# Kernel tuning notes

Hardware: AMD Instinct MI355X
Metric: run time of the kernel (lower is better)

## Reference

```python
import jax, jax.numpy as jnp
import numpy as np

N_NODES = 262144
N_EDGES = 4194304
NUM_GRAPHS = 1024
K = 2          # k clusters / particles
D = 4          # particle_latent_dim
D_Q = D // 2   # position part of latent


def setup_inputs() -> dict:
    key = jax.random.key(0)
    ks = jax.random.split(key, 20)
    w = lambda i, shape: 0.1 * jax.random.normal(ks[i], shape, jnp.float32)
    return {
        "x": jax.random.normal(ks[0], (N_NODES, 4), jnp.float32),
        "pos": jax.random.normal(ks[1], (N_NODES, 3), jnp.float32),
        "edge_index": jax.random.randint(ks[2], (2, N_EDGES), 0, N_NODES),
        "batch": jnp.sort(jax.random.randint(ks[3], (N_NODES,), 0, NUM_GRAPHS)),
        "enc_w1": w(4, (9, 16)), "enc_b1": jnp.zeros((16,), jnp.float32),
        "enc_w2": w(5, (16, 16)), "enc_b2": jnp.zeros((16,), jnp.float32),
        "pool_w": w(6, (16, K)), "pool_b": jnp.zeros((K,), jnp.float32),
        "toz_w": w(7, (16, D)), "toz_b": jnp.zeros((D,), jnp.float32),
        "vp_w1": w(8, (1, 32)), "vp_b1": jnp.zeros((32,), jnp.float32),
        "vp_w2": w(9, (32, 1)), "vp_b2": jnp.zeros((1,), jnp.float32),
        "bridge_w": w(10, (K * D, 8 * 4)), "bridge_b": jnp.zeros((8 * 4,), jnp.float32),
    }


def reference(x, pos, edge_index, batch,
              enc_w1, enc_b1, enc_w2, enc_b2,
              pool_w, pool_b, toz_w, toz_b,
              vp_w1, vp_b1, vp_w2, vp_b2,
              bridge_w, bridge_b):
    src = edge_index[0]  # j (source)
    dst = edge_index[1]  # i (target, PyG default flow)

    # --- EquiLayer: edge gather -> small MLP message -> mean scatter ---
    rel_pos = pos[src] - pos[dst]
    dist = jnp.linalg.norm(rel_pos, axis=-1, keepdims=True)       # [E,1]
    feat = jnp.concatenate([x[dst], x[src], dist], axis=-1)       # [E,9]
    msg = jax.nn.silu(feat @ enc_w1 + enc_b1) @ enc_w2 + enc_b2   # [E,16]
    agg = jax.ops.segment_sum(msg, dst, num_segments=N_NODES)     # [N,16]
    cnt = jax.ops.segment_sum(jnp.ones((msg.shape[0], 1), msg.dtype), dst,
                              num_segments=N_NODES)
    h = jax.nn.relu(agg / jnp.maximum(cnt, 1.0))                  # [N,16]

    # --- softmax-weighted scatter pooling over graphs ---
    s = jax.nn.softmax(h @ pool_w + pool_b, axis=-1)              # [N,K]
    weighted = s[:, :, None] * h[:, None, :]                      # [N,K,16]
    pooled = jax.ops.segment_sum(weighted, batch, num_segments=NUM_GRAPHS)  # [B,K,16]
    z = pooled @ toz_w + toz_b                                    # [B,K,D]

    # --- decode ---
    recon = (z.reshape(z.shape[0], -1) @ bridge_w + bridge_b).reshape(-1, 8, 4)

    # --- pairwise potential + forces on position part of latent ---
    iu0, iu1 = np.triu_indices(K, 1)

    def potential(q):
        diff = q[:, :, None, :] - q[:, None, :, :]
        d = jnp.sqrt(jnp.sum(diff * diff, axis=-1) + 1e-6)        # [B,K,K]
        d_flat = d[:, iu0, iu1][..., None]                        # [B,P,1]
        v = jax.nn.softplus(d_flat @ vp_w1 + vp_b1) @ vp_w2 + vp_b2
        return v.sum(axis=1)                                      # [B,1]

    q = z[..., :D_Q]
    V = potential(q)
    forces = -jax.grad(lambda qq: potential(qq).sum())(q)
    return recon, z, s, forces, V
```

## Files before the change

kernel.cpp:

```cpp
#include <hip/hip_runtime.h>
#include <math.h>

#define N_NODES   262144
#define N_EDGES   4194304
#define NUM_GRAPHS 1024
#define NBKT      256
#define BNODE     1024
#define CAPK      17408
#define NBLK      256
#define EPB       16384
#define SEGCAP    112

typedef _Float16 h8 __attribute__((ext_vector_type(8)));

static __device__ __forceinline__ float fast_rcp(float v) {
    return __builtin_amdgcn_rcpf(v);
}

__global__ __launch_bounds__(1024) void bin_pack_kernel(
    const int* __restrict__ ei, const float* __restrict__ x,
    const float* __restrict__ pos,
    int* __restrict__ cnts, int* __restrict__ staged,
    h8* __restrict__ xp, float* __restrict__ pooled)
{
    __shared__ int cnt[NBKT], rcnt[NBKT], lbase[NBKT];
    __shared__ int wsum[4];
    __shared__ int stage[EPB];
    int tid = threadIdx.x;
    if (tid < NBKT) { cnt[tid] = 0; rcnt[tid] = 0; }
    __syncthreads();

    {
        int n0 = blockIdx.x * 1024 + tid;
        float4 xv = *(const float4*)(x + 4*n0);
        h8 o;
        o[0] = (_Float16)xv.x; o[1] = (_Float16)xv.y;
        o[2] = (_Float16)xv.z; o[3] = (_Float16)xv.w;
        o[4] = (_Float16)pos[3*n0+0]; o[5] = (_Float16)pos[3*n0+1];
        o[6] = (_Float16)pos[3*n0+2]; o[7] = (_Float16)0.0f;
        xp[n0] = o;
        if (blockIdx.x < 32) pooled[blockIdx.x*1024 + tid] = 0.0f;
    }

    int base = blockIdx.x * EPB;
    const int4* d4 = (const int4*)(ei + N_EDGES + base);
    const int4* s4 = (const int4*)(ei + base);
    int4 dv[4];
    #pragma unroll
    for (int i = 0; i < 4; ++i) {
        dv[i] = d4[i*1024 + tid];
        atomicAdd(&cnt[dv[i].x >> 10], 1);
        atomicAdd(&cnt[dv[i].y >> 10], 1);
        atomicAdd(&cnt[dv[i].z >> 10], 1);
        atomicAdd(&cnt[dv[i].w >> 10], 1);
    }
    __syncthreads();

    int lane = tid & 63, wid = tid >> 6;
    if (tid < NBKT) {
        int inc = cnt[tid];
        #pragma unroll
        for (int o = 1; o < 64; o <<= 1) {
            int t = __shfl_up(inc, o);
            if (lane >= o) inc += t;
        }
        if (lane == 63) wsum[wid] = inc;
        cnt[tid] = inc;
    }
    __syncthreads();
    if (tid < NBKT) {
        int inc  = cnt[tid];
        int prev = __shfl_up(inc, 1);
        int excl = (lane == 0) ? 0 : prev;
        int wb = 0;
        #pragma unroll
        for (int w = 0; w < 4; ++w) if (w < wid) wb += wsum[w];
        lbase[tid] = wb + excl;
    }
    __syncthreads();

    #pragma unroll
    for (int i = 0; i < 4; ++i) {
        int4 sv = s4[i*1024 + tid];
        int d, s, bk, r;
        d = dv[i].x; s = sv.x; bk = d >> 10; r = atomicAdd(&rcnt[bk], 1);
        stage[lbase[bk] + r] = ((d & 1023) << 18) | s;
        d = dv[i].y; s = sv.y; bk = d >> 10; r = atomicAdd(&rcnt[bk], 1);
        stage[lbase[bk] + r] = ((d & 1023) << 18) | s;
        d = dv[i].z; s = sv.z; bk = d >> 10; r = atomicAdd(&rcnt[bk], 1);
        stage[lbase[bk] + r] = ((d & 1023) << 18) | s;
        d = dv[i].w; s = sv.w; bk = d >> 10; r = atomicAdd(&rcnt[bk], 1);
        stage[lbase[bk] + r] = ((d & 1023) << 18) | s;
    }
    __syncthreads();

    int sub = tid & 31, grp = tid >> 5;
    #pragma unroll
    for (int pass = 0; pass < NBKT/32; ++pass) {
        int bk  = pass*32 + grp;
        int c2  = rcnt[bk];
        int lb  = lbase[bk];
        if (c2 > SEGCAP) c2 = SEGCAP;
        size_t sb = ((size_t)bk*NBLK + blockIdx.x)*SEGCAP;
        for (int k = sub; k < c2; k += 32)
            staged[sb + k] = stage[lb + k];
        if (sub == 0) cnts[bk*NBLK + blockIdx.x] = c2;
    }
}

static __device__ __forceinline__ void edge_contrib(
    const float* __restrict__ sw1, const float* __restrict__ hd,
    float4 xs, float dist, float* __restrict__ acc)
{
    float h[16];
    #pragma unroll
    for (int j4 = 0; j4 < 4; ++j4) {
        float4 w = *(const float4*)&sw1[4*16 + 4*j4];
        h[4*j4+0] = fmaf(xs.x, w.x, hd[4*j4+0]);
        h[4*j4+1] = fmaf(xs.x, w.y, hd[4*j4+1]);
        h[4*j4+2] = fmaf(xs.x, w.z, hd[4*j4+2]);
        h[4*j4+3] = fmaf(xs.x, w.w, hd[4*j4+3]);
    }
    #pragma unroll
    for (int j4 = 0; j4 < 4; ++j4) {
        float4 w = *(const float4*)&sw1[5*16 + 4*j4];
        h[4*j4+0] = fmaf(xs.y, w.x, h[4*j4+0]);
        h[4*j4+1] = fmaf(xs.y, w.y, h[4*j4+1]);
        h[4*j4+2] = fmaf(xs.y, w.z, h[4*j4+2]);
        h[4*j4+3] = fmaf(xs.y, w.w, h[4*j4+3]);
    }
    #pragma unroll
    for (int j4 = 0; j4 < 4; ++j4) {
        float4 w = *(const float4*)&sw1[6*16 + 4*j4];
        h[4*j4+0] = fmaf(xs.z, w.x, h[4*j4+0]);
        h[4*j4+1] = fmaf(xs.z, w.y, h[4*j4+1]);
        h[4*j4+2] = fmaf(xs.z, w.z, h[4*j4+2]);
        h[4*j4+3] = fmaf(xs.z, w.w, h[4*j4+3]);
    }
    #pragma unroll
    for (int j4 = 0; j4 < 4; ++j4) {
        float4 w = *(const float4*)&sw1[7*16 + 4*j4];
        h[4*j4+0] = fmaf(xs.w, w.x, h[4*j4+0]);
        h[4*j4+1] = fmaf(xs.w, w.y, h[4*j4+1]);
        h[4*j4+2] = fmaf(xs.w, w.z, h[4*j4+2]);
        h[4*j4+3] = fmaf(xs.w, w.w, h[4*j4+3]);
    }
    #pragma unroll
    for (int j4 = 0; j4 < 4; ++j4) {
        float4 w = *(const float4*)&sw1[8*16 + 4*j4];
        h[4*j4+0] = fmaf(dist, w.x, h[4*j4+0]);
        h[4*j4+1] = fmaf(dist, w.y, h[4*j4+1]);
        h[4*j4+2] = fmaf(dist, w.z, h[4*j4+2]);
        h[4*j4+3] = fmaf(dist, w.w, h[4*j4+3]);
    }
    #pragma unroll
    for (int j = 0; j < 16; ++j) {
        float sg = fast_rcp(1.0f + __expf(-h[j]));
        acc[j] = fmaf(h[j], sg, acc[j]);
    }
}

__global__ __launch_bounds__(1024, 4) void fused_node_kernel(
    const h8* __restrict__ xp,
    const int* __restrict__ cnts, const int* __restrict__ staged,
    const int* __restrict__ batch,
    const float* __restrict__ w1, const float* __restrict__ b1,
    const float* __restrict__ w2, const float* __restrict__ b2,
    const float* __restrict__ pw, const float* __restrict__ pb,
    float* __restrict__ s_out, float* __restrict__ pooled)
{
    __shared__ union {
        int   esrc[CAPK];
        float accbuf[CAPK];
    } u;
    __shared__ int   ldeg[BNODE];
    __shared__ int   perm[BNODE];
    __shared__ int   scnt[NBLK];
    __shared__ int   dhist[64];
    __shared__ int   wsum[16];
    __shared__ __align__(16) float sw1[144];
    __shared__ float sb1[16];
    __shared__ __align__(16) float sw2[256];
    __shared__ float sb2[16];
    __shared__ float spw[32];
    __shared__ float spb[2];

    int tid = threadIdx.x;
    int bkt = blockIdx.x;
    if (tid < 144) sw1[tid] = w1[tid];
    if (tid >= 144 && tid < 160) sb1[tid - 144] = b1[tid - 144];
    if (tid >= 160 && tid < 176) sb2[tid - 160] = b2[tid - 160];
    if (tid >= 176 && tid < 208) spw[tid - 176] = pw[tid - 176];
    if (tid >= 208 && tid < 210) spb[tid - 208] = pb[tid - 208];
    if (tid >= 256 && tid < 512) sw2[tid - 256] = w2[tid - 256];
    if (tid >= 512 && tid < 768) scnt[tid - 512] = cnts[bkt*NBLK + (tid - 512)];
    if (tid >= 768 && tid < 832) dhist[tid - 768] = 0;
    ldeg[tid] = 0;
    __syncthreads();

    int lane = tid & 63, wid = tid >> 6;
    int nb0  = bkt * BNODE;

    for (int s = wid; s < NBLK; s += 16) {
        int c = scnt[s];
        const int* seg = staged + ((size_t)bkt*NBLK + s)*SEGCAP;
        for (int i = lane; i < c; i += 64)
            atomicAdd(&ldeg[seg[i] >> 18], 1);
    }
    __syncthreads();

    int dg  = ldeg[tid];
    int inc = dg;
    #pragma unroll
    for (int o = 1; o < 64; o <<= 1) {
        int t = __shfl_up(inc, o);
        if (lane >= o) inc += t;
    }
    if (lane == 63) wsum[wid] = inc;
    __syncthreads();
    int wb = 0;
    #pragma unroll
    for (int w = 0; w < 16; ++w) if (w < wid) wb += wsum[w];
    int r0 = wb + inc - dg;
    ldeg[tid] = r0;
    __syncthreads();

    for (int s = wid; s < NBLK; s += 16) {
        int c = scnt[s];
        const int* seg = staged + ((size_t)bkt*NBLK + s)*SEGCAP;
        for (int i = lane; i < c; i += 64) {
            int p = seg[i];
            int r = atomicAdd(&ldeg[p >> 18], 1);
            if (r < CAPK) u.esrc[r] = p & 0x3FFFF;
        }
    }
    int db = dg < 63 ? dg : 63;
    atomicAdd(&dhist[db], 1);
    __syncthreads();

    if (tid < 64) {
        int c  = dhist[tid];
        int i2 = c;
        #pragma unroll
        for (int o = 1; o < 64; o <<= 1) {
            int t2 = __shfl_up(i2, o);
            if (lane >= o) i2 += t2;
        }
        dhist[tid] = i2 - c;
    }
    __syncthreads();
    int rank = atomicAdd(&dhist[db], 1);
    perm[rank] = (r0 << 10) | tid;
    __syncthreads();

    int pk  = perm[tid];
    int v   = pk & 1023;
    int r0v = pk >> 10;
    int dgv = ldeg[v] - r0v;
    h8 rd = xp[nb0 + v];
    float4 xd = make_float4((float)rd[0], (float)rd[1], (float)rd[2], (float)rd[3]);
    float pdx = (float)rd[4], pdy = (float)rd[5], pdz = (float)rd[6];

    float hd[16];
    #pragma unroll
    for (int j = 0; j < 16; ++j) hd[j] = sb1[j];
    #pragma unroll
    for (int j4 = 0; j4 < 4; ++j4) {
        float4 w0 = *(const float4*)&sw1[0*16 + 4*j4];
        float4 w1r = *(const float4*)&sw1[1*16 + 4*j4];
        float4 w2r = *(const float4*)&sw1[2*16 + 4*j4];
        float4 w3r = *(const float4*)&sw1[3*16 + 4*j4];
        hd[4*j4+0] = fmaf(xd.x, w0.x, hd[4*j4+0]);
        hd[4*j4+1] = fmaf(xd.x, w0.y, hd[4*j4+1]);
        hd[4*j4+2] = fmaf(xd.x, w0.z, hd[4*j4+2]);
        hd[4*j4+3] = fmaf(xd.x, w0.w, hd[4*j4+3]);
        hd[4*j4+0] = fmaf(xd.y, w1r.x, hd[4*j4+0]);
        hd[4*j4+1] = fmaf(xd.y, w1r.y, hd[4*j4+1]);
        hd[4*j4+2] = fmaf(xd.y, w1r.z, hd[4*j4+2]);
        hd[4*j4+3] = fmaf(xd.y, w1r.w, hd[4*j4+3]);
        hd[4*j4+0] = fmaf(xd.z, w2r.x, hd[4*j4+0]);
        hd[4*j4+1] = fmaf(xd.z, w2r.y, hd[4*j4+1]);
        hd[4*j4+2] = fmaf(xd.z, w2r.z, hd[4*j4+2]);
        hd[4*j4+3] = fmaf(xd.z, w2r.w, hd[4*j4+3]);
        hd[4*j4+0] = fmaf(xd.w, w3r.x, hd[4*j4+0]);
        hd[4*j4+1] = fmaf(xd.w, w3r.y, hd[4*j4+1]);
        hd[4*j4+2] = fmaf(xd.w, w3r.z, hd[4*j4+2]);
        hd[4*j4+3] = fmaf(xd.w, w3r.w, hd[4*j4+3]);
    }

    float acc[16];
    #pragma unroll
    for (int j = 0; j < 16; ++j) acc[j] = 0.0f;

    int k = 0;
    for (; k + 2 <= dgv; k += 2) {
        int s0 = u.esrc[r0v + k];
        int s1 = u.esrc[r0v + k + 1];
        h8 e0 = xp[s0];
        h8 e1 = xp[s1];

        float4 a0 = make_float4((float)e0[0], (float)e0[1], (float)e0[2], (float)e0[3]);
        float dx0 = (float)e0[4] - pdx, dy0 = (float)e0[5] - pdy, dz0 = (float)e0[6] - pdz;
        float dist0 = sqrtf(fmaf(dx0, dx0, fmaf(dy0, dy0, dz0*dz0)));
        edge_contrib(sw1, hd, a0, dist0, acc);

        float4 a1 = make_float4((float)e1[0], (float)e1[1], (float)e1[2], (float)e1[3]);
        float dx1 = (float)e1[4] - pdx, dy1 = (float)e1[5] - pdy, dz1 = (float)e1[6] - pdz;
        float dist1 = sqrtf(fmaf(dx1, dx1, fmaf(dy1, dy1, dz1*dz1)));
        edge_contrib(sw1, hd, a1, dist1, acc);
    }
    if (k < dgv) {
        int s0 = u.esrc[r0v + k];
        h8 e0 = xp[s0];
        float4 a0 = make_float4((float)e0[0], (float)e0[1], (float)e0[2], (float)e0[3]);
        float dx0 = (float)e0[4] - pdx, dy0 = (float)e0[5] - pdy, dz0 = (float)e0[6] - pdz;
        float dist0 = sqrtf(fmaf(dx0, dx0, fmaf(dy0, dy0, dz0*dz0)));
        edge_contrib(sw1, hd, a0, dist0, acc);
    }
    __syncthreads();

    #pragma unroll
    for (int j = 0; j < 16; ++j) u.accbuf[v*17 + j] = acc[j];
    __syncthreads();

    int n = nb0 + tid;
    int dgc = ldeg[tid] - r0;
    float c = (float)dgc;
    float inv = fast_rcp(fmaxf(c, 1.0f));
    float h[16];
    #pragma unroll
    for (int j = 0; j < 16; ++j) h[j] = c * sb2[j];
    #pragma unroll
    for (int i = 0; i < 16; ++i) {
        float f = u.accbuf[tid*17 + i];
        #pragma unroll
        for (int j4 = 0; j4 < 4; ++j4) {
            float4 w = *(const float4*)&sw2[i*16 + 4*j4];
            h[4*j4+0] = fmaf(f, w.x, h[4*j4+0]);
            h[4*j4+1] = fmaf(f, w.y, h[4*j4+1]);
            h[4*j4+2] = fmaf(f, w.z, h[4*j4+2]);
            h[4*j4+3] = fmaf(f, w.w, h[4*j4+3]);
        }
    }
    #pragma unroll
    for (int j = 0; j < 16; ++j) h[j] = fmaxf(h[j] * inv, 0.0f);

    float l0 = spb[0], l1 = spb[1];
    #pragma unroll
    for (int j = 0; j < 16; ++j) {
        l0 = fmaf(h[j], spw[2*j+0], l0);
        l1 = fmaf(h[j], spw[2*j+1], l1);
    }
    float m = fmaxf(l0, l1);
    float e0 = __expf(l0 - m), e1 = __expf(l1 - m);
    float r = fast_rcp(e0 + e1);
    float s0 = e0 * r, s1 = e1 * r;
    s_out[2*n+0] = s0;
    s_out[2*n+1] = s1;

    float w[32];
    #pragma unroll
    for (int j = 0; j < 16; ++j) { w[j] = s0 * h[j]; w[16+j] = s1 * h[j]; }

    int b = batch[n];
    #pragma unroll
    for (int o = 1; o < 64; o <<= 1) {
        int bn = __shfl_down(b, o);
        bool take = (lane + o < 64) && (bn == b);
        #pragma unroll
        for (int cc = 0; cc < 32; ++cc) {
            float vn = __shfl_down(w[cc], o);
            if (take) w[cc] += vn;
        }
    }
    int bp = __shfl_up(b, 1);
    if (lane == 0 || bp != b) {
        float* pg = pooled + 32*b;
        #pragma unroll
        for (int cc = 0; cc < 32; ++cc) unsafeAtomicAdd(pg + cc, w[cc]);
    }
}

__global__ __launch_bounds__(256) void graph_kernel(
    const float* __restrict__ pooled,
    const float* __restrict__ toz_w, const float* __restrict__ toz_b,
    const float* __restrict__ vp_w1, const float* __restrict__ vp_b1,
    const float* __restrict__ vp_w2, const float* __restrict__ vp_b2,
    const float* __restrict__ bridge_w, const float* __restrict__ bridge_b,
    float* __restrict__ out_recon, float* __restrict__ out_z,
    float* __restrict__ out_forces, float* __restrict__ out_V)
{
    int g = blockIdx.x * 256 + threadIdx.x;
    if (g >= NUM_GRAPHS) return;

    const float* P = pooled + 32*g;
    float z[8];
    #pragma unroll
    for (int k = 0; k < 2; ++k) {
        #pragma unroll
        for (int d = 0; d < 4; ++d) {
            float a = toz_b[d];
            #pragma unroll
            for (int i = 0; i < 16; ++i) a = fmaf(P[16*k+i], toz_w[4*i+d], a);
            z[4*k+d] = a;
        }
    }
    #pragma unroll
    for (int i = 0; i < 8; ++i) out_z[8*g+i] = z[i];

    #pragma unroll
    for (int j = 0; j < 32; ++j) {
        float a = bridge_b[j];
        #pragma unroll
        for (int i = 0; i < 8; ++i) a = fmaf(z[i], bridge_w[32*i+j], a);
        out_recon[32*g+j] = a;
    }

    float d0 = z[0]-z[4], d1 = z[1]-z[5];
    float dd = sqrtf(d0*d0 + d1*d1 + 1e-6f);

    float V = vp_b2[0];
    float dV = 0.0f;
    #pragma unroll
    for (int j = 0; j < 32; ++j) {
        float w1 = vp_w1[j];
        float t  = fmaf(dd, w1, vp_b1[j]);
        float et = __expf(t);
        float sp = __logf(1.0f + et);
        float sg = et / (1.0f + et);
        float w2 = vp_w2[j];
        V  = fmaf(sp, w2, V);
        dV = fmaf(sg * w1, w2, dV);
    }
    out_V[g] = V;

    float scale = dV / dd;
    float gx = scale * d0, gy = scale * d1;
    out_forces[4*g+0] = -gx;
    out_forces[4*g+1] = -gy;
    out_forces[4*g+2] =  gx;
    out_forces[4*g+3] =  gy;
}

extern "C" void kernel_launch(void* const* d_in, const int* in_sizes, int n_in,
                              void* d_out, int out_size, void* d_ws, size_t ws_size,
                              hipStream_t stream) {
    const float* x        = (const float*)d_in[0];
    const float* pos      = (const float*)d_in[1];
    const int*   ei       = (const int*)  d_in[2];
    const int*   batch    = (const int*)  d_in[3];
    const float* enc_w1   = (const float*)d_in[4];
    const float* enc_b1   = (const float*)d_in[5];
    const float* enc_w2   = (const float*)d_in[6];
    const float* enc_b2   = (const float*)d_in[7];
    const float* pool_w   = (const float*)d_in[8];
    const float* pool_b   = (const float*)d_in[9];
    const float* toz_w    = (const float*)d_in[10];
    const float* toz_b    = (const float*)d_in[11];
    const float* vp_w1    = (const float*)d_in[12];
    const float* vp_b1    = (const float*)d_in[13];
    const float* vp_w2    = (const float*)d_in[14];
    const float* vp_b2    = (const float*)d_in[15];
    const float* bridge_w = (const float*)d_in[16];
    const float* bridge_b = (const float*)d_in[17];

    int*   cnts   = (int*)d_ws;
    float* pooled = (float*)d_ws + NBKT*NBLK;
    int*   staged = (int*)d_ws + NBKT*NBLK + 32768;
    h8*    xp     = (h8*)(staged + (size_t)NBKT*NBLK*SEGCAP);

    float* out        = (float*)d_out;
    float* out_recon  = out;
    float* out_z      = out_recon + 1024*32;
    float* out_s      = out_z + 1024*8;
    float* out_forces = out_s + (size_t)N_NODES*2;
    float* out_V      = out_forces + 1024*4;

    bin_pack_kernel<<<NBLK, 1024, 0, stream>>>(ei, x, pos, cnts, staged, xp, pooled);
    fused_node_kernel<<<NBKT, 1024, 0, stream>>>(
        xp, cnts, staged, batch,
        enc_w1, enc_b1, enc_w2, enc_b2, pool_w, pool_b, out_s, pooled);
    graph_kernel<<<NUM_GRAPHS/256, 256, 0, stream>>>(
        pooled, toz_w, toz_b, vp_w1, vp_b1, vp_w2, vp_b2,
        bridge_w, bridge_b, out_recon, out_z, out_forces, out_V);
}
```

Before: 206.9 us.

## Split node buckets across two blocks and use two threads per node

The fused node kernel now launches two blocks per 1024-node bucket, each handling 512 nodes, so the grid doubles to 512 blocks and the shared edge list shrinks by about half. Within a block, each node's edges are split between two adjacent threads (even/odd edges) and their partial sums are combined with a lane shuffle before the node MLP and pooling. This is meant to raise occupancy and spread the edge-gather work across more threads. In exchange, each block must scan the full staged segment list twice and discard the half it does not own, and half the threads idle in the node epilogue.

```diff
diff --git a/kernel.cpp b/kernel.cpp
--- a/kernel.cpp
+++ b/kernel.cpp
@@ -5,8 +5,8 @@
 #define N_EDGES   4194304
 #define NUM_GRAPHS 1024
 #define NBKT      256
-#define BNODE     1024
-#define CAPK      17408
+#define HNODE     512
+#define CAPH      8960
 #define NBLK      256
 #define EPB       16384
 #define SEGCAP    112
@@ -170,14 +170,14 @@
     float* __restrict__ s_out, float* __restrict__ pooled)
 {
     __shared__ union {
-        int   esrc[CAPK];
-        float accbuf[CAPK];
+        int   esrc[CAPH];
+        float accbuf[CAPH];
     } u;
-    __shared__ int   ldeg[BNODE];
-    __shared__ int   perm[BNODE];
+    __shared__ int   ldeg[HNODE];
+    __shared__ int   perm[HNODE];
     __shared__ int   scnt[NBLK];
     __shared__ int   dhist[64];
-    __shared__ int   wsum[16];
+    __shared__ int   wsum[8];
     __shared__ __align__(16) float sw1[144];
     __shared__ float sb1[16];
     __shared__ __align__(16) float sw2[256];
@@ -185,8 +185,9 @@
     __shared__ float spw[32];
     __shared__ float spb[2];
 
-    int tid = threadIdx.x;
-    int bkt = blockIdx.x;
+    int tid  = threadIdx.x;
+    int bkt  = blockIdx.x >> 1;
+    int half = blockIdx.x & 1;
     if (tid < 144) sw1[tid] = w1[tid];
     if (tid >= 144 && tid < 160) sb1[tid - 144] = b1[tid - 144];
     if (tid >= 160 && tid < 176) sb2[tid - 160] = b2[tid - 160];
@@ -195,47 +196,60 @@
     if (tid >= 256 && tid < 512) sw2[tid - 256] = w2[tid - 256];
     if (tid >= 512 && tid < 768) scnt[tid - 512] = cnts[bkt*NBLK + (tid - 512)];
     if (tid >= 768 && tid < 832) dhist[tid - 768] = 0;
-    ldeg[tid] = 0;
+    if (tid < HNODE) ldeg[tid] = 0;
     __syncthreads();
 
     int lane = tid & 63, wid = tid >> 6;
-    int nb0  = bkt * BNODE;
-
-    for (int s = wid; s < NBLK; s += 16) {
-        int c = scnt[s];
-        const int* seg = staged + ((size_t)bkt*NBLK + s)*SEGCAP;
-        for (int i = lane; i < c; i += 64)
-            atomicAdd(&ldeg[seg[i] >> 18], 1);
-    }
-    __syncthreads();
-
-    int dg  = ldeg[tid];
-    int inc = dg;
-    #pragma unroll
-    for (int o = 1; o < 64; o <<= 1) {
-        int t = __shfl_up(inc, o);
-        if (lane >= o) inc += t;
-    }
-    if (lane == 63) wsum[wid] = inc;
-    __syncthreads();
-    int wb = 0;
-    #pragma unroll
-    for (int w = 0; w < 16; ++w) if (w < wid) wb += wsum[w];
-    int r0 = wb + inc - dg;
-    ldeg[tid] = r0;
-    __syncthreads();
+    int nb0  = bkt * 1024 + half * HNODE;
 
     for (int s = wid; s < NBLK; s += 16) {
         int c = scnt[s];
         const int* seg = staged + ((size_t)bkt*NBLK + s)*SEGCAP;
         for (int i = lane; i < c; i += 64) {
-            int p = seg[i];
-            int r = atomicAdd(&ldeg[p >> 18], 1);
-            if (r < CAPK) u.esrc[r] = p & 0x3FFFF;
-        }
-    }
-    int db = dg < 63 ? dg : 63;
-    atomicAdd(&dhist[db], 1);
+            int lo = seg[i] >> 18;
+            if ((lo >> 9) == half) atomicAdd(&ldeg[lo & 511], 1);
+        }
+    }
+    __syncthreads();
+
+    int dg = 0, r0 = 0;
+    if (tid < HNODE) {
+        dg = ldeg[tid];
+        int inc = dg;
+        #pragma unroll
+        for (int o = 1; o < 64; o <<= 1) {
+            int t = __shfl_up(inc, o);
+            if (lane >= o) inc += t;
+        }
+        if (lane == 63) wsum[wid] = inc;
+        r0 = inc - dg;
+    }
+    __syncthreads();
+    if (tid < HNODE) {
+        int wb = 0;
+        #pragma unroll
+        for (int w = 0; w < 8; ++w) if (w < wid) wb += wsum[w];
+        r0 += wb;
+        ldeg[tid] = r0;
+    }
+    __syncthreads();
+
+    for (int s = wid; s < NBLK; s += 16) {
+        int c = scnt[s];
+        const int* seg = staged + ((size_t)bkt*NBLK + s)*SEGCAP;
+        for (int i = lane; i < c; i += 64) {
+            int p  = seg[i];
+            int lo = p >> 18;
+            if ((lo >> 9) == half) {
+                int r = atomicAdd(&ldeg[lo & 511], 1);
+                if (r < CAPH) u.esrc[r] = p & 0x3FFFF;
+            }
+        }
+    }
+    if (tid < HNODE) {
+        int db = dg < 63 ? dg : 63;
+        atomicAdd(&dhist[db], 1);
+    }
     __syncthreads();
 
     if (tid < 64) {
@@ -249,14 +263,19 @@
         dhist[tid] = i2 - c;
     }
     __syncthreads();
-    int rank = atomicAdd(&dhist[db], 1);
-    perm[rank] = (r0 << 10) | tid;
-    __syncthreads();
-
-    int pk  = perm[tid];
-    int v   = pk & 1023;
-    int r0v = pk >> 10;
-    int dgv = ldeg[v] - r0v;
+    if (tid < HNODE) {
+        int db   = dg < 63 ? dg : 63;
+        int rank = atomicAdd(&dhist[db], 1);
+        perm[rank] = (r0 << 9) | tid;
+    }
+    __syncthreads();
+
+    int idx   = tid >> 1;
+    int par   = tid & 1;
+    int pk    = perm[idx];
+    int v     = pk & 511;
+    int r0v   = pk >> 9;
+    int dgv   = ldeg[v] - r0v;
     h8 rd = xp[nb0 + v];
     float4 xd = make_float4((float)rd[0], (float)rd[1], (float)rd[2], (float)rd[3]);
     float pdx = (float)rd[4], pdy = (float)rd[5], pdz = (float)rd[6];
@@ -292,10 +311,10 @@
     #pragma unroll
     for (int j = 0; j < 16; ++j) acc[j] = 0.0f;
 
-    int k = 0;
-    for (; k + 2 <= dgv; k += 2) {
+    int k = par;
+    for (; k + 2 < dgv; k += 4) {
         int s0 = u.esrc[r0v + k];
-        int s1 = u.esrc[r0v + k + 1];
+        int s1 = u.esrc[r0v + k + 2];
         h8 e0 = xp[s0];
         h8 e1 = xp[s1];
 
@@ -320,64 +339,70 @@
     __syncthreads();
 
     #pragma unroll
-    for (int j = 0; j < 16; ++j) u.accbuf[v*17 + j] = acc[j];
-    __syncthreads();
-
-    int n = nb0 + tid;
-    int dgc = ldeg[tid] - r0;
-    float c = (float)dgc;
-    float inv = fast_rcp(fmaxf(c, 1.0f));
-    float h[16];
-    #pragma unroll
-    for (int j = 0; j < 16; ++j) h[j] = c * sb2[j];
-    #pragma unroll
-    for (int i = 0; i < 16; ++i) {
-        float f = u.accbuf[tid*17 + i];
-        #pragma unroll
-        for (int j4 = 0; j4 < 4; ++j4) {
-            float4 w = *(const float4*)&sw2[i*16 + 4*j4];
-            h[4*j4+0] = fmaf(f, w.x, h[4*j4+0]);
-            h[4*j4+1] = fmaf(f, w.y, h[4*j4+1]);
-            h[4*j4+2] = fmaf(f, w.z, h[4*j4+2]);
-            h[4*j4+3] = fmaf(f, w.w, h[4*j4+3]);
-        }
-    }
-    #pragma unroll
-    for (int j = 0; j < 16; ++j) h[j] = fmaxf(h[j] * inv, 0.0f);
-
-    float l0 = spb[0], l1 = spb[1];
-    #pragma unroll
-    for (int j = 0; j < 16; ++j) {
-        l0 = fmaf(h[j], spw[2*j+0], l0);
-        l1 = fmaf(h[j], spw[2*j+1], l1);
-    }
-    float m = fmaxf(l0, l1);
-    float e0 = __expf(l0 - m), e1 = __expf(l1 - m);
-    float r = fast_rcp(e0 + e1);
-    float s0 = e0 * r, s1 = e1 * r;
-    s_out[2*n+0] = s0;
-    s_out[2*n+1] = s1;
-
-    float w[32];
-    #pragma unroll
-    for (int j = 0; j < 16; ++j) { w[j] = s0 * h[j]; w[16+j] = s1 * h[j]; }
-
-    int b = batch[n];
-    #pragma unroll
-    for (int o = 1; o < 64; o <<= 1) {
-        int bn = __shfl_down(b, o);
-        bool take = (lane + o < 64) && (bn == b);
-        #pragma unroll
-        for (int cc = 0; cc < 32; ++cc) {
-            float vn = __shfl_down(w[cc], o);
-            if (take) w[cc] += vn;
-        }
-    }
-    int bp = __shfl_up(b, 1);
-    if (lane == 0 || bp != b) {
-        float* pg = pooled + 32*b;
-        #pragma unroll
-        for (int cc = 0; cc < 32; ++cc) unsafeAtomicAdd(pg + cc, w[cc]);
+    for (int j = 0; j < 16; ++j) acc[j] += __shfl_xor(acc[j], 1);
+    if (par == 0) {
+        #pragma unroll
+        for (int j = 0; j < 16; ++j) u.accbuf[v*17 + j] = acc[j];
+    }
+    __syncthreads();
+
+    if (tid < HNODE) {
+        int n = nb0 + tid;
+        int dgc = ldeg[tid] - r0;
+        float c = (float)dgc;
+        float inv = fast_rcp(fmaxf(c, 1.0f));
+        float h[16];
+        #pragma unroll
+        for (int j = 0; j < 16; ++j) h[j] = c * sb2[j];
+        #pragma unroll
+        for (int i = 0; i < 16; ++i) {
+            float f = u.accbuf[tid*17 + i];
+            #pragma unroll
+            for (int j4 = 0; j4 < 4; ++j4) {
+                float4 w = *(const float4*)&sw2[i*16 + 4*j4];
+                h[4*j4+0] = fmaf(f, w.x, h[4*j4+0]);
+                h[4*j4+1] = fmaf(f, w.y, h[4*j4+1]);
+                h[4*j4+2] = fmaf(f, w.z, h[4*j4+2]);
+                h[4*j4+3] = fmaf(f, w.w, h[4*j4+3]);
+            }
+        }
+        #pragma unroll
+        for (int j = 0; j < 16; ++j) h[j] = fmaxf(h[j] * inv, 0.0f);
+
+        float l0 = spb[0], l1 = spb[1];
+        #pragma unroll
+        for (int j = 0; j < 16; ++j) {
+            l0 = fmaf(h[j], spw[2*j+0], l0);
+            l1 = fmaf(h[j], spw[2*j+1], l1);
+        }
+        float m = fmaxf(l0, l1);
+        float e0 = __expf(l0 - m), e1 = __expf(l1 - m);
+        float r = fast_rcp(e0 + e1);
+        float s0 = e0 * r, s1 = e1 * r;
+        s_out[2*n+0] = s0;
+        s_out[2*n+1] = s1;
+
+        float w[32];
+        #pragma unroll
+        for (int j = 0; j < 16; ++j) { w[j] = s0 * h[j]; w[16+j] = s1 * h[j]; }
+
+        int b = batch[n];
+        #pragma unroll
+        for (int o = 1; o < 64; o <<= 1) {
+            int bn = __shfl_down(b, o);
+            bool take = (lane + o < 64) && (bn == b);
+            #pragma unroll
+            for (int cc = 0; cc < 32; ++cc) {
+                float vn = __shfl_down(w[cc], o);
+                if (take) w[cc] += vn;
+            }
+        }
+        int bp = __shfl_up(b, 1);
+        if (lane == 0 || bp != b) {
+            float* pg = pooled + 32*b;
+            #pragma unroll
+            for (int cc = 0; cc < 32; ++cc) unsafeAtomicAdd(pg + cc, w[cc]);
+        }
     }
 }
 
@@ -477,7 +502,7 @@
     float* out_V      = out_forces + 1024*4;
 
     bin_pack_kernel<<<NBLK, 1024, 0, stream>>>(ei, x, pos, cnts, staged, xp, pooled);
-    fused_node_kernel<<<NBKT, 1024, 0, stream>>>(
+    fused_node_kernel<<<NBKT*2, 1024, 0, stream>>>(
         xp, cnts, staged, batch,
         enc_w1, enc_b1, enc_w2, enc_b2, pool_w, pool_b, out_s, pooled);
     graph_kernel<<<NUM_GRAPHS/256, 256, 0, stream>>>(
```

Result: slower. 334.6 us (+61.7%).
